# Kernel tuning notes

Measured on AMD Instinct MI355X. Metric: run time of the kernel, lower is better.

Reference implementation:

```python
import jax, jax.numpy as jnp
import numpy as np

N = 8192
IN_FEAT = 256
OUT_FEAT = 128
N_EDGES = 262144
NEG_SLOPE = 0.2
NORM_EPS = 1e-12  # torch F.normalize default eps


def setup_inputs() -> dict:
    key = jax.random.key(0)
    k1, k2, k3, k4 = jax.random.split(key, 4)
    features = jax.random.normal(k1, (N, IN_FEAT), dtype=jnp.float32)
    # xavier_normal scale for W and a (matches nn.init.xavier_normal_ statistics)
    w_std = float(np.sqrt(2.0 / (IN_FEAT + OUT_FEAT)))
    a_std = float(np.sqrt(2.0 / (2 * OUT_FEAT + 1)))
    W = jax.random.normal(k2, (IN_FEAT, OUT_FEAT), dtype=jnp.float32) * w_std
    a = jax.random.normal(k3, (2 * OUT_FEAT, 1), dtype=jnp.float32) * a_std
    edge_index = jax.random.randint(k4, (2, N_EDGES), 0, N, dtype=jnp.int64)
    return {"features": features, "W": W, "a": a, "edge_index": edge_index}


def reference(features, W, a, edge_index):
    n = features.shape[0]
    # to_dense_adj: scatter-add ones into dense [N, N] (padded to N as in module)
    adj = jnp.zeros((n, n), dtype=features.dtype).at[edge_index[0], edge_index[1]].add(1.0)
    HW = features @ W  # [N, F]
    f = HW.shape[1]
    # pairwise_features_masked @ a == adj_ij * (HW_i . a[:F] + HW_j . a[F:])
    s = HW @ a[:f, 0]  # [N] source-side score
    t = HW @ a[f:, 0]  # [N] target-side score
    e = (s[:, None] + t[None, :]) * adj  # [N, N], mask applied before leakyReLU
    e = jnp.where(e > 0, e, NEG_SLOPE * e)  # leaky_relu(0.2)
    # F.normalize(e, dim=0): L2-normalize each column
    col_norm = jnp.sqrt(jnp.sum(e * e, axis=0, keepdims=True))
    alpha = e / jnp.maximum(col_norm, NORM_EPS)
    # dropout p=0 -> identity
    return alpha @ HW  # [N, F]
```

## Files before the change

### kernel.cpp

```cpp
#include <hip/hip_runtime.h>

#define NN 8192
#define NE 262144
#define CAP 128

__global__ __launch_bounds__(256) void k_fused1(const float* __restrict__ feat,
                                                const float* __restrict__ Wm,
                                                float* __restrict__ HW,
                                                float* __restrict__ s,
                                                float* __restrict__ t,
                                                const float* __restrict__ a,
                                                const int* __restrict__ src,
                                                const int* __restrict__ dst,
                                                int* __restrict__ cnt,
                                                int* __restrict__ col) {
    const int b = blockIdx.x;
    const int tid = threadIdx.x;
    if (b >= 512) {
        const int e = (b - 512) * 256 + tid;
        const int i = src[e];
        const int pos = atomicAdd(&cnt[i], 1);
        if (pos < CAP) col[i * CAP + pos] = dst[e];
        return;
    }
    __shared__ float fs[16 * 256];
    __shared__ float red[2][4][8];
    const int f = tid & 127;
    const int rh = tid >> 7;
    const int row0 = b * 16;
    for (int idx = tid * 4; idx < 16 * 256; idx += 256 * 4) {
        *(float4*)&fs[idx] = *(const float4*)&feat[row0 * 256 + idx];
    }
    __syncthreads();
    float acc[8];
#pragma unroll
    for (int r = 0; r < 8; ++r) acc[r] = 0.f;
    const float* fsr = fs + rh * 8 * 256;
    for (int k = 0; k < 256; k += 4) {
        const float w0 = Wm[(k + 0) * 128 + f];
        const float w1 = Wm[(k + 1) * 128 + f];
        const float w2 = Wm[(k + 2) * 128 + f];
        const float w3 = Wm[(k + 3) * 128 + f];
#pragma unroll
        for (int r = 0; r < 8; ++r) {
            const float4 fv = *(const float4*)&fsr[r * 256 + k];
            acc[r] += fv.x * w0 + fv.y * w1 + fv.z * w2 + fv.w * w3;
        }
    }
#pragma unroll
    for (int r = 0; r < 8; ++r) {
        HW[(row0 + rh * 8 + r) * 128 + f] = acc[r];
    }
    const float as_ = a[f];
    const float at_ = a[128 + f];
    const int w = tid >> 6;
    const int lane = tid & 63;
#pragma unroll
    for (int r = 0; r < 8; ++r) {
        float vs = acc[r] * as_;
        float vt = acc[r] * at_;
        for (int off = 32; off; off >>= 1) {
            vs += __shfl_xor(vs, off);
            vt += __shfl_xor(vt, off);
        }
        if (lane == 0) { red[0][w][r] = vs; red[1][w][r] = vt; }
    }
    __syncthreads();
    if (tid < 8)       s[row0 + tid] = red[0][0][tid] + red[0][1][tid];
    else if (tid < 16) s[row0 + tid] = red[0][2][tid - 8] + red[0][3][tid - 8];
    else if (tid < 24) t[row0 + (tid - 16)] = red[1][0][tid - 16] + red[1][1][tid - 16];
    else if (tid < 32) t[row0 + 8 + (tid - 24)] = red[1][2][tid - 24] + red[1][3][tid - 24];
}

__global__ __launch_bounds__(256) void k_dupnorm(const int* __restrict__ cnt,
                                                 const int* __restrict__ col,
                                                 const float* __restrict__ s,
                                                 const float* __restrict__ t,
                                                 float* __restrict__ norm2) {
    __shared__ int cs[4][CAP];
    const int lane = threadIdx.x & 63;
    const int w = threadIdx.x >> 6;
    const int row = blockIdx.x * 4 + w;
    const int deg = min(cnt[row], CAP);
    int jA = -1, jB = -1;
    if (lane < deg) jA = col[row * CAP + lane];
    if (64 + lane < deg) jB = col[row * CAP + 64 + lane];
    cs[w][lane] = jA;
    cs[w][64 + lane] = jB;
    __syncthreads();
    const float si = s[row];
    float lrA = 0.f, lrB = 0.f;
    if (jA >= 0) { const float x = si + t[jA]; lrA = x > 0.f ? x : 0.2f * x; }
    if (jB >= 0) { const float x = si + t[jB]; lrB = x > 0.f ? x : 0.2f * x; }
    int cA = 0, cB = 0;
    for (int q = 0; q < deg; ++q) {
        const int v = cs[w][q];
        cA += (v == jA);
        cB += (v == jB);
    }
    if (jA >= 0) atomicAdd(&norm2[jA], (float)cA * lrA * lrA);
    if (jB >= 0) atomicAdd(&norm2[jB], (float)cB * lrB * lrB);
}

__global__ __launch_bounds__(256) void k_spmm(const int* __restrict__ cnt,
                                              const int* __restrict__ col,
                                              const float* __restrict__ s,
                                              const float* __restrict__ t,
                                              const float* __restrict__ norm2,
                                              const float* __restrict__ HW,
                                              float* __restrict__ out) {
    const int lane = threadIdx.x & 63;
    const int w = threadIdx.x >> 6;
    const int row = blockIdx.x * 2 + (w >> 1);
    const int f = (w & 1) * 64 + lane;
    const int deg = min(cnt[row], CAP);
    const float si = s[row];
    int j0 = 0;
    float c0 = 0.f;
    if (lane < deg) {
        j0 = col[row * CAP + lane];
        const float x = si + t[j0];
        const float lr = x > 0.f ? x : 0.2f * x;
        c0 = lr / fmaxf(sqrtf(norm2[j0]), 1e-12f);
    }
    float a0 = 0.f, a1 = 0.f, a2 = 0.f, a3 = 0.f;
    const int d0 = min(deg, 64);
    int e = 0;
    for (; e + 3 < d0; e += 4) {
        const int ja = __shfl(j0, e), jb = __shfl(j0, e + 1);
        const int jc = __shfl(j0, e + 2), jd = __shfl(j0, e + 3);
        const float ca = __shfl(c0, e), cb = __shfl(c0, e + 1);
        const float cc = __shfl(c0, e + 2), cd = __shfl(c0, e + 3);
        a0 += ca * HW[ja * 128 + f];
        a1 += cb * HW[jb * 128 + f];
        a2 += cc * HW[jc * 128 + f];
        a3 += cd * HW[jd * 128 + f];
    }
    for (; e < d0; ++e) {
        a0 += __shfl(c0, e) * HW[__shfl(j0, e) * 128 + f];
    }
    if (deg > 64) {
        int j1 = 0;
        float c1 = 0.f;
        if (64 + lane < deg) {
            j1 = col[row * CAP + 64 + lane];
            const float x = si + t[j1];
            const float lr = x > 0.f ? x : 0.2f * x;
            c1 = lr / fmaxf(sqrtf(norm2[j1]), 1e-12f);
        }
        const int d1 = deg - 64;
        for (e = 0; e < d1; ++e) {
            a0 += __shfl(c1, e) * HW[__shfl(j1, e) * 128 + f];
        }
    }
    out[row * 128 + f] = a0 + a1 + a2 + a3;
}

extern "C" void kernel_launch(void* const* d_in, const int* in_sizes, int n_in,
                              void* d_out, int out_size, void* d_ws, size_t ws_size,
                              hipStream_t stream) {
    const float* feat = (const float*)d_in[0];
    const float* Wm = (const float*)d_in[1];
    const float* a = (const float*)d_in[2];
    const int* edges = (const int*)d_in[3];
    const int* src = edges;
    const int* dst = edges + NE;
    float* out = (float*)d_out;

    float* HW = (float*)d_ws;
    float* s = HW + NN * 128;
    float* t = s + NN;
    float* norm2 = t + NN;
    int* cnt = (int*)(norm2 + NN);
    int* col = cnt + NN;

    hipMemsetAsync(norm2, 0, 2 * NN * sizeof(float), stream);

    k_fused1<<<512 + NE / 256, 256, 0, stream>>>(feat, Wm, HW, s, t, a, src, dst, cnt, col);
    k_dupnorm<<<NN / 4, 256, 0, stream>>>(cnt, col, s, t, norm2);
    k_spmm<<<NN / 2, 256, 0, stream>>>(cnt, col, s, t, norm2, HW, out);
}
```

Before: 125.6 us.

## Store HW intermediate in bf16 and remap GEMM threads to drop block reduction

HW is now written as bf16 and the SpMM gather reads bf16 values, halving the bytes moved by the random row gathers. The GEMM now gives each wave 4 rows and 2 features per thread, so the s/t dot-products reduce within a single wave and the shared-memory reduction and second barrier go away. The cost is lower precision in the aggregated output, since HW is rounded to bf16 before the weighted sum.

```diff
diff --git a/kernel.cpp b/kernel.cpp
--- a/kernel.cpp
+++ b/kernel.cpp
@@ -1,4 +1,5 @@
 #include <hip/hip_runtime.h>
+#include <hip/hip_bf16.h>
 
 #define NN 8192
 #define NE 262144
@@ -6,12 +7,12 @@
 
 __global__ __launch_bounds__(256) void k_fused1(const float* __restrict__ feat,
                                                 const float* __restrict__ Wm,
-                                                float* __restrict__ HW,
-                                                float* __restrict__ s,
-                                                float* __restrict__ t,
                                                 const float* __restrict__ a,
                                                 const int* __restrict__ src,
                                                 const int* __restrict__ dst,
+                                                __hip_bfloat16* __restrict__ HWb,
+                                                float* __restrict__ s,
+                                                float* __restrict__ t,
                                                 int* __restrict__ cnt,
                                                 int* __restrict__ col) {
     const int b = blockIdx.x;
@@ -24,52 +25,45 @@
         return;
     }
     __shared__ float fs[16 * 256];
-    __shared__ float red[2][4][8];
-    const int f = tid & 127;
-    const int rh = tid >> 7;
+    const int fq = tid & 63;
+    const int w = tid >> 6;
     const int row0 = b * 16;
-    for (int idx = tid * 4; idx < 16 * 256; idx += 256 * 4) {
+    for (int idx = tid * 4; idx < 16 * 256; idx += 256 * 4)
         *(float4*)&fs[idx] = *(const float4*)&feat[row0 * 256 + idx];
-    }
     __syncthreads();
-    float acc[8];
+    float acc[4][2] = {};
+    const float* fsr = fs + w * 4 * 256;
+    for (int k = 0; k < 256; k += 4) {
+        float4 fv[4];
 #pragma unroll
-    for (int r = 0; r < 8; ++r) acc[r] = 0.f;
-    const float* fsr = fs + rh * 8 * 256;
-    for (int k = 0; k < 256; k += 4) {
-        const float w0 = Wm[(k + 0) * 128 + f];
-        const float w1 = Wm[(k + 1) * 128 + f];
-        const float w2 = Wm[(k + 2) * 128 + f];
-        const float w3 = Wm[(k + 3) * 128 + f];
+        for (int r = 0; r < 4; ++r) fv[r] = *(const float4*)&fsr[r * 256 + k];
+        float wv[4][2];
 #pragma unroll
-        for (int r = 0; r < 8; ++r) {
-            const float4 fv = *(const float4*)&fsr[r * 256 + k];
-            acc[r] += fv.x * w0 + fv.y * w1 + fv.z * w2 + fv.w * w3;
+        for (int i = 0; i < 4; ++i) {
+            wv[i][0] = Wm[(k + i) * 128 + fq];
+            wv[i][1] = Wm[(k + i) * 128 + fq + 64];
+        }
+#pragma unroll
+        for (int r = 0; r < 4; ++r) {
+            acc[r][0] += fv[r].x * wv[0][0] + fv[r].y * wv[1][0] + fv[r].z * wv[2][0] + fv[r].w * wv[3][0];
+            acc[r][1] += fv[r].x * wv[0][1] + fv[r].y * wv[1][1] + fv[r].z * wv[2][1] + fv[r].w * wv[3][1];
         }
     }
+    const float aS0 = a[fq], aS1 = a[fq + 64];
+    const float aT0 = a[128 + fq], aT1 = a[192 + fq];
 #pragma unroll
-    for (int r = 0; r < 8; ++r) {
-        HW[(row0 + rh * 8 + r) * 128 + f] = acc[r];
-    }
-    const float as_ = a[f];
-    const float at_ = a[128 + f];
-    const int w = tid >> 6;
-    const int lane = tid & 63;
-#pragma unroll
-    for (int r = 0; r < 8; ++r) {
-        float vs = acc[r] * as_;
-        float vt = acc[r] * at_;
+    for (int r = 0; r < 4; ++r) {
+        const int row = row0 + w * 4 + r;
+        HWb[row * 128 + fq] = __float2bfloat16(acc[r][0]);
+        HWb[row * 128 + fq + 64] = __float2bfloat16(acc[r][1]);
+        float vs = acc[r][0] * aS0 + acc[r][1] * aS1;
+        float vt = acc[r][0] * aT0 + acc[r][1] * aT1;
         for (int off = 32; off; off >>= 1) {
             vs += __shfl_xor(vs, off);
             vt += __shfl_xor(vt, off);
         }
-        if (lane == 0) { red[0][w][r] = vs; red[1][w][r] = vt; }
+        if (fq == 0) { s[row] = vs; t[row] = vt; }
     }
-    __syncthreads();
-    if (tid < 8)       s[row0 + tid] = red[0][0][tid] + red[0][1][tid];
-    else if (tid < 16) s[row0 + tid] = red[0][2][tid - 8] + red[0][3][tid - 8];
-    else if (tid < 24) t[row0 + (tid - 16)] = red[1][0][tid - 16] + red[1][1][tid - 16];
-    else if (tid < 32) t[row0 + 8 + (tid - 24)] = red[1][2][tid - 24] + red[1][3][tid - 24];
 }
 
 __global__ __launch_bounds__(256) void k_dupnorm(const int* __restrict__ cnt,
@@ -107,7 +101,7 @@
                                               const float* __restrict__ s,
                                               const float* __restrict__ t,
                                               const float* __restrict__ norm2,
-                                              const float* __restrict__ HW,
+                                              const __hip_bfloat16* __restrict__ HWb,
                                               float* __restrict__ out) {
     const int lane = threadIdx.x & 63;
     const int w = threadIdx.x >> 6;
@@ -131,14 +125,13 @@
         const int jc = __shfl(j0, e + 2), jd = __shfl(j0, e + 3);
         const float ca = __shfl(c0, e), cb = __shfl(c0, e + 1);
         const float cc = __shfl(c0, e + 2), cd = __shfl(c0, e + 3);
-        a0 += ca * HW[ja * 128 + f];
-        a1 += cb * HW[jb * 128 + f];
-        a2 += cc * HW[jc * 128 + f];
-        a3 += cd * HW[jd * 128 + f];
+        a0 += ca * __bfloat162float(HWb[ja * 128 + f]);
+        a1 += cb * __bfloat162float(HWb[jb * 128 + f]);
+        a2 += cc * __bfloat162float(HWb[jc * 128 + f]);
+        a3 += cd * __bfloat162float(HWb[jd * 128 + f]);
     }
-    for (; e < d0; ++e) {
-        a0 += __shfl(c0, e) * HW[__shfl(j0, e) * 128 + f];
-    }
+    for (; e < d0; ++e)
+        a0 += __shfl(c0, e) * __bfloat162float(HWb[__shfl(j0, e) * 128 + f]);
     if (deg > 64) {
         int j1 = 0;
         float c1 = 0.f;
@@ -149,9 +142,8 @@
             c1 = lr / fmaxf(sqrtf(norm2[j1]), 1e-12f);
         }
         const int d1 = deg - 64;
-        for (e = 0; e < d1; ++e) {
-            a0 += __shfl(c1, e) * HW[__shfl(j1, e) * 128 + f];
-        }
+        for (e = 0; e < d1; ++e)
+            a0 += __shfl(c1, e) * __bfloat162float(HWb[__shfl(j1, e) * 128 + f]);
     }
     out[row * 128 + f] = a0 + a1 + a2 + a3;
 }
@@ -167,8 +159,8 @@
     const int* dst = edges + NE;
     float* out = (float*)d_out;
 
-    float* HW = (float*)d_ws;
-    float* s = HW + NN * 128;
+    __hip_bfloat16* HWb = (__hip_bfloat16*)d_ws;
+    float* s = (float*)(HWb + NN * 128);
     float* t = s + NN;
     float* norm2 = t + NN;
     int* cnt = (int*)(norm2 + NN);
@@ -176,7 +168,7 @@
 
     hipMemsetAsync(norm2, 0, 2 * NN * sizeof(float), stream);
 
-    k_fused1<<<512 + NE / 256, 256, 0, stream>>>(feat, Wm, HW, s, t, a, src, dst, cnt, col);
+    k_fused1<<<512 + NE / 256, 256, 0, stream>>>(feat, Wm, a, src, dst, HWb, s, t, cnt, col);
     k_dupnorm<<<NN / 4, 256, 0, stream>>>(cnt, col, s, t, norm2);
-    k_spmm<<<NN / 2, 256, 0, stream>>>(cnt, col, s, t, norm2, HW, out);
+    k_spmm<<<NN / 2, 256, 0, stream>>>(cnt, col, s, t, norm2, HWb, out);
 }
```

Measured after the change: 124.3 us. No clear change (-1.0%).
